# Performance work log

Measured on AMD Instinct MI355X. Metric: run time of the kernel, lower is better.

The kernel has to match this reference:

```python
import jax, jax.numpy as jnp
import numpy as np

D_MODEL = 1024
NUM_HEADS = 16
ROPE_THETA = 10000.0


def setup_inputs() -> dict:
    key = jax.random.key(0)
    ks = jax.random.split(key, 5)
    B, S, D = 4, 2048, D_MODEL
    scale = 1.0 / np.sqrt(D)
    return {
        "x": jax.random.normal(ks[0], (B, S, D), dtype=jnp.float32),
        "Wq": jax.random.normal(ks[1], (D, D), dtype=jnp.float32) * scale,
        "Wk": jax.random.normal(ks[2], (D, D), dtype=jnp.float32) * scale,
        "Wv": jax.random.normal(ks[3], (D, D), dtype=jnp.float32) * scale,
        "Wo": jax.random.normal(ks[4], (D, D), dtype=jnp.float32) * scale,
        "token_positions": jnp.arange(S, dtype=jnp.int32),
    }


def _rope(x, pos, theta=ROPE_THETA):
    # x: (b, h, s, d); interleaved-pair rotary embedding
    d = x.shape[-1]
    inv_freq = 1.0 / (theta ** (jnp.arange(0, d, 2, dtype=jnp.float32) / d))  # (d/2,)
    ang = pos.astype(jnp.float32)[:, None] * inv_freq[None, :]  # (s, d/2)
    cos, sin = jnp.cos(ang), jnp.sin(ang)
    x1, x2 = x[..., ::2], x[..., 1::2]
    out = jnp.stack([x1 * cos - x2 * sin, x1 * sin + x2 * cos], axis=-1)
    return out.reshape(x.shape)


def reference(x, Wq, Wk, Wv, Wo, token_positions):
    B, S, D = x.shape
    H = NUM_HEADS
    dh = D // H
    # torch nn.Linear(bias=False): y = x @ W.T
    q = jnp.einsum('bsd,ed->bse', x, Wq).reshape(B, S, H, dh).transpose(0, 2, 1, 3)
    k = jnp.einsum('bsd,ed->bse', x, Wk).reshape(B, S, H, dh).transpose(0, 2, 1, 3)
    v = jnp.einsum('bsd,ed->bse', x, Wv).reshape(B, S, H, dh).transpose(0, 2, 1, 3)
    q = _rope(q, token_positions)
    k = _rope(k, token_positions)
    scores = jnp.einsum('bhqd,bhkd->bhqk', q, k) / jnp.sqrt(jnp.array(dh, x.dtype))
    causal = jnp.tril(jnp.ones((S, S), dtype=bool))
    scores = jnp.where(causal, scores, jnp.array(-jnp.inf, scores.dtype))
    probs = jax.nn.softmax(scores, axis=-1)
    attn = jnp.einsum('bhqk,bhkd->bhqd', probs, v)  # (b, h, s, dh)
    attn = attn.transpose(0, 2, 1, 3).reshape(B, S, D)
    return jnp.einsum('bsd,ed->bse', attn, Wo)
```

## Files before the change

kernel.cpp:

```cpp
#include <hip/hip_runtime.h>
#include <hip/hip_bf16.h>
#include <stdint.h>

#define S_LEN 2048
#define BATCH 4
#define NH    16
#define DH    64
#define DM    1024
#define MTOT  (BATCH*S_LEN)

typedef short bf16x8 __attribute__((ext_vector_type(8)));
typedef float f32x4 __attribute__((ext_vector_type(4)));
typedef uint32_t u32x4 __attribute__((ext_vector_type(4)));

__device__ __forceinline__ uint16_t f2bf(float f) {
  union { float f; uint32_t i; } c; c.f = f;
  uint32_t r = c.i + 0x7fffu + ((c.i >> 16) & 1u);
  return (uint16_t)(r >> 16);
}
__device__ __forceinline__ float bf2f(uint16_t u) {
  union { uint32_t i; float f; } c; c.i = ((uint32_t)u) << 16; return c.f;
}

__device__ __forceinline__ uint32_t cvt_pk_bf16(float a, float b) {
  uint32_t r;
  asm("v_cvt_pk_bf16_f32 %0, %1, %2" : "=v"(r) : "v"(a), "v"(b));
  return r;
}

__device__ __forceinline__ void async_copy16(void* lds, const void* g) {
  __builtin_amdgcn_global_load_lds(
      (const __attribute__((address_space(1))) void*)g,
      (__attribute__((address_space(3))) void*)lds, 16, 0, 0);
}

__global__ __launch_bounds__(256) void cvt_f32_bf16(const float* __restrict__ in,
                                                    uint16_t* __restrict__ out, int n4) {
  int stride = gridDim.x * blockDim.x;
  for (int i = blockIdx.x * blockDim.x + threadIdx.x; i < n4; i += stride) {
    float4 v = ((const float4*)in)[i];
    ushort4 o;
    o.x = f2bf(v.x); o.y = f2bf(v.y); o.z = f2bf(v.z); o.w = f2bf(v.w);
    ((ushort4*)out)[i] = o;
  }
}

__global__ __launch_bounds__(256) void cvt_w4(const float* __restrict__ wq,
                                              const float* __restrict__ wk,
                                              const float* __restrict__ wv,
                                              const float* __restrict__ wo,
                                              uint16_t* __restrict__ out) {
  const int sel = blockIdx.y;
  const float* src = sel == 0 ? wq : sel == 1 ? wk : sel == 2 ? wv : wo;
  uint16_t* dst = out + (size_t)sel * DM * DM;
  const int n4 = DM * DM / 4;
  const int stride = gridDim.x * blockDim.x;
  for (int i = blockIdx.x * blockDim.x + threadIdx.x; i < n4; i += stride) {
    float4 v = ((const float4*)src)[i];
    ushort4 o;
    o.x = f2bf(v.x); o.y = f2bf(v.y); o.z = f2bf(v.z); o.w = f2bf(v.w);
    ((ushort4*)dst)[i] = o;
  }
}

template<int MODE, int BN>
__global__ __launch_bounds__(256) void gemm_bt(const uint16_t* __restrict__ A,
                                               const uint16_t* __restrict__ Bw,
                                               void* __restrict__ outp,
                                               const int* __restrict__ pos) {
  constexpr int K = DM;
  constexpr int NT = K / 32;
  constexpr int WC = BN / 2;
  constexpr int NF = WC / 16;
  __shared__ __align__(16) uint16_t lA[3][128 * 32];
  __shared__ __align__(16) uint16_t lB[3][BN * 32];
  const int tid = threadIdx.x;
  const int w = tid >> 6, lane = tid & 63;
  const int l15 = lane & 15, lhi = lane >> 4;
  const int wr = w >> 1, wc = w & 1;

  const int nx = gridDim.x, nwg = nx * gridDim.y;
  const int flat = blockIdx.y * nx + blockIdx.x;
  const int wg = (flat & 7) * (nwg >> 3) + (flat >> 3);
  const int bm = (wg / nx) * 128, bn = (wg % nx) * BN;

  const int srow = tid >> 2;
  const int cb = (tid & 3) * 16;

  auto stage = [&](int b, int t) {
    const int k0 = t * 32;
#pragma unroll
    for (int i = 0; i < 2; ++i)
      async_copy16((char*)lA[b] + i * 4096 + w * 1024,
                   (const char*)A + ((size_t)(bm + i * 64 + srow) * K + k0) * 2 + cb);
#pragma unroll
    for (int i = 0; i < BN / 64; ++i)
      async_copy16((char*)lB[b] + i * 4096 + w * 1024,
                   (const char*)Bw + ((size_t)(bn + i * 64 + srow) * K + k0) * 2 + cb);
  };

  f32x4 acc[4][NF] = {};

  stage(0, 0);
  stage(1, 1);
  if constexpr (BN == 128) asm volatile("s_waitcnt vmcnt(4)" ::: "memory");
  else                     asm volatile("s_waitcnt vmcnt(3)" ::: "memory");
  __builtin_amdgcn_s_barrier();
  __builtin_amdgcn_sched_barrier(0);

  int cur = 0;
  for (int t = 0; t < NT; ++t) {
    const bool pre = (t + 2 < NT);
    int bnext = cur + 2; if (bnext >= 3) bnext -= 3;
    if (pre) stage(bnext, t + 2);

    bf16x8 af[4], bfr[NF];
#pragma unroll
    for (int mf = 0; mf < 4; ++mf)
      af[mf] = *(const bf16x8*)((const char*)lA[cur] +
                                (wr * 64 + mf * 16 + l15) * 64 + lhi * 16);
#pragma unroll
    for (int nf = 0; nf < NF; ++nf)
      bfr[nf] = *(const bf16x8*)((const char*)lB[cur] +
                                 (wc * WC + nf * 16 + l15) * 64 + lhi * 16);
    __builtin_amdgcn_s_setprio(1);
#pragma unroll
    for (int mf = 0; mf < 4; ++mf)
#pragma unroll
      for (int nf = 0; nf < NF; ++nf)
        acc[mf][nf] = __builtin_amdgcn_mfma_f32_16x16x32_bf16(af[mf], bfr[nf], acc[mf][nf], 0, 0, 0);
    __builtin_amdgcn_s_setprio(0);

    if (pre) {
      if constexpr (BN == 128) asm volatile("s_waitcnt vmcnt(4)" ::: "memory");
      else                     asm volatile("s_waitcnt vmcnt(3)" ::: "memory");
    } else {
      asm volatile("s_waitcnt vmcnt(0)" ::: "memory");
    }
    __builtin_amdgcn_s_barrier();
    __builtin_amdgcn_sched_barrier(0);
    cur = cur + 1 == 3 ? 0 : cur + 1;
  }

  if (MODE == 0) {
    const int tsel = bn >> 10;
    uint16_t* out = (uint16_t*)outp + (size_t)tsel * ((size_t)MTOT * DM);
    if (tsel < 2) {
      const float l2t_32 = 0.41524101186092074f;
      const float qsc = tsel == 0 ? 0.18033688011112042f : 1.0f;
#pragma unroll
      for (int mf = 0; mf < 4; ++mf) {
        float ps[4];
#pragma unroll
        for (int r = 0; r < 4; ++r) {
          const int m = bm + wr * 64 + mf * 16 + lhi * 4 + r;
          ps[r] = (float)pos[m & (S_LEN - 1)];
        }
#pragma unroll
        for (int nf = 0; nf < NF; ++nf) {
          const int n = bn + wc * WC + nf * 16 + l15;
          const int e = n & 1023;
          const int h = e >> 6, d = e & 63;
          const float inv = __builtin_amdgcn_exp2f(-(float)(d >> 1) * l2t_32);
#pragma unroll
          for (int r = 0; r < 4; ++r) {
            const int m = bm + wr * 64 + mf * 16 + lhi * 4 + r;
            const int b = m >> 11, s = m & (S_LEN - 1);
            const float v = acc[mf][nf][r];
            const float p = __shfl_xor(v, 1);
            const float ang = ps[r] * inv;
            const float cs = __cosf(ang) * qsc, sn = __sinf(ang) * qsc;
            const float val = (l15 & 1) ? (p * sn + v * cs) : (v * cs - p * sn);
            out[(((size_t)(b * NH + h) * S_LEN + s) << 6) + d] = f2bf(val);
          }
        }
      }
    } else {
#pragma unroll
      for (int mf = 0; mf < 4; ++mf)
#pragma unroll
        for (int nf = 0; nf < NF; ++nf)
#pragma unroll
          for (int r = 0; r < 4; ++r) {
            const int m = bm + wr * 64 + mf * 16 + lhi * 4 + r;
            const int n = bn + wc * WC + nf * 16 + l15;
            const int b = m >> 11, s = m & (S_LEN - 1);
            const int e = n & 1023;
            const int h = e >> 6, d = e & 63;
            out[(((size_t)(b * NH + h) * S_LEN + s) << 6) + d] = f2bf(acc[mf][nf][r]);
          }
    }
  } else {
    float* out = (float*)outp;
#pragma unroll
    for (int mf = 0; mf < 4; ++mf)
#pragma unroll
      for (int nf = 0; nf < NF; ++nf)
#pragma unroll
        for (int r = 0; r < 4; ++r) {
          const int m = bm + wr * 64 + mf * 16 + lhi * 4 + r;
          const int n = bn + wc * WC + nf * 16 + l15;
          out[(size_t)m * DM + n] = acc[mf][nf][r];
        }
  }
}

__global__ __launch_bounds__(256) void transpose_v(const uint16_t* __restrict__ v,
                                                   uint16_t* __restrict__ vt) {
  __shared__ uint16_t t[64 * 65];
  const int bh = blockIdx.y, s0 = blockIdx.x * 64;
  const uint16_t* vb = v + (size_t)bh * S_LEN * 64 + (size_t)s0 * 64;
  uint16_t* ob = vt + (size_t)bh * 64 * S_LEN + s0;
  for (int o = threadIdx.x; o < 64 * 64; o += 256) {
    const int r = o >> 6, c = o & 63;
    t[c * 65 + r] = vb[(size_t)r * 64 + c];
  }
  __syncthreads();
  for (int o = threadIdx.x; o < 64 * 64; o += 256) {
    const int d = o >> 6, p = o & 63;
    const int sp = (p & 32) | (((p >> 2) & 3) << 3) | (((p >> 4) & 1) << 2) | (p & 3);
    ob[(size_t)d * S_LEN + sp] = t[d * 65 + p];
  }
}

__global__ __launch_bounds__(512, 4) void attn_kernel(const uint16_t* __restrict__ q,
                                                      const uint16_t* __restrict__ kk,
                                                      const uint16_t* __restrict__ vt,
                                                      uint16_t* __restrict__ o) {
  const int bh = blockIdx.y;
  const int p = blockIdx.x;
  const int tid = threadIdx.x;
  const int w = __builtin_amdgcn_readfirstlane(tid >> 6);
  const int lane = tid & 63;
  const int l15 = lane & 15, lhi = lane >> 4;
  const uint16_t* qb = q + (size_t)bh * S_LEN * DH;
  const uint16_t* kb = kk + (size_t)bh * S_LEN * DH;
  const uint16_t* vb = vt + (size_t)bh * DH * S_LEN;

  __shared__ uint16_t lK[2][128 * 64];
  __shared__ uint16_t lV[2][64 * 128];

  const int krow_l = lane >> 3;
  const int scK = (lane & 7) ^ krow_l;
  const int vrow_l = lane >> 4;

  auto stage = [&](int b, int t) {
    const int k0 = t * 128;
#pragma unroll
    for (int i = 0; i < 2; ++i) {
      const int krow = w * 16 + i * 8 + krow_l;
      async_copy16((char*)lK[b] + w * 2048 + i * 1024 + lane * 16,
                   (const char*)kb + ((size_t)(k0 + krow) * 64 + scK * 8) * 2);
      const int vd = w * 8 + i * 4 + vrow_l;
      const int scV = (lane & 15) ^ (vd & 15);
      async_copy16((char*)lV[b] + w * 2048 + i * 1024 + lane * 16,
                   (const char*)vb + ((size_t)vd * S_LEN + k0 + scV * 8) * 2);
    }
  };

  stage(0, 0);
  asm volatile("s_waitcnt vmcnt(0)" ::: "memory");
  __syncthreads();

  int cur = 0;
  const int b_out = bh >> 4, h_out = bh & 15;

  for (int s = 0; s < 2; ++s) {
    const int qtile = s ? p : (15 - p);
    const int q0 = qtile * 128 + w * 16;

    bf16x8 qf[2];
#pragma unroll
    for (int c = 0; c < 2; ++c)
      qf[c] = *(const bf16x8*)(qb + (size_t)(q0 + l15) * DH + c * 32 + lhi * 8);

    f32x4 oa[4] = {};
    float mr = -1e30f, lr = 0.f;

    const int nt = qtile + 1;
    for (int t = 0; t < nt; ++t) {
      if (t + 1 < nt) stage(cur ^ 1, t + 1);
      else if (s == 0) stage(cur ^ 1, 0);

      const bool diag = (t == qtile);
      const int fMf = diag ? w : 7;
      const int fE  = diag ? (w | 1) : 7;
      const int cE  = diag ? (w >> 1) : 3;

      f32x4 sf[8];
      __builtin_amdgcn_s_setprio(1);
#pragma unroll
      for (int f = 0; f < 8; ++f) {
        f32x4 z = {0.f, 0.f, 0.f, 0.f};
        if (f <= fMf) {
          const int kr = f * 16 + l15;
          const char* kbase = (const char*)lK[cur] + kr * 128;
          bf16x8 kf0 = *(const bf16x8*)(kbase + ((lhi ^ (kr & 7)) << 4));
          bf16x8 kf1 = *(const bf16x8*)(kbase + (((4 + lhi) ^ (kr & 7)) << 4));
          z = __builtin_amdgcn_mfma_f32_16x16x32_bf16(kf0, qf[0], z, 0, 0, 0);
          z = __builtin_amdgcn_mfma_f32_16x16x32_bf16(kf1, qf[1], z, 0, 0, 0);
        }
        sf[f] = z;
      }
      __builtin_amdgcn_s_setprio(0);

      if (diag) {
        const int qrow = q0 + l15;
        const int k0 = t * 128;
#pragma unroll
        for (int f = 0; f < 8; ++f)
          if (f <= fE)
#pragma unroll
            for (int r = 0; r < 4; ++r) {
              const int kv = k0 + f * 16 + lhi * 4 + r;
              if (kv > qrow) sf[f][r] = -1e30f;
            }
      }

      float pm = -1e30f;
#pragma unroll
      for (int f = 0; f < 8; ++f)
        if (f <= fE)
#pragma unroll
          for (int r = 0; r < 4; ++r) pm = fmaxf(pm, sf[f][r]);
      pm = fmaxf(pm, __shfl_xor(pm, 16));
      pm = fmaxf(pm, __shfl_xor(pm, 32));

      if (!__all(pm <= mr + 8.0f)) {
        const float mn = fmaxf(mr, pm);
        const float resc = __builtin_amdgcn_exp2f(mr - mn);
        mr = mn;
        lr *= resc;
#pragma unroll
        for (int r = 0; r < 4; ++r) {
          const float rb = __shfl(resc, (lhi << 2) + r);
#pragma unroll
          for (int df = 0; df < 4; ++df) oa[df][r] *= rb;
        }
      }

      float rs = 0.f;
#pragma unroll
      for (int f = 0; f < 8; ++f)
        if (f <= fE)
#pragma unroll
          for (int r = 0; r < 4; ++r) {
            const float pv = __builtin_amdgcn_exp2f(sf[f][r] - mr);
            sf[f][r] = pv;
            rs += pv;
          }
      rs += __shfl_xor(rs, 16);
      rs += __shfl_xor(rs, 32);
      lr += rs;

#pragma unroll
      for (int c = 0; c < 4; ++c) {
        if (c <= cE) {
          u32x4 u;
          u.x = cvt_pk_bf16(sf[2 * c][0], sf[2 * c][1]);
          u.y = cvt_pk_bf16(sf[2 * c][2], sf[2 * c][3]);
          u.z = cvt_pk_bf16(sf[2 * c + 1][0], sf[2 * c + 1][1]);
          u.w = cvt_pk_bf16(sf[2 * c + 1][2], sf[2 * c + 1][3]);
          bf16x8 pa = __builtin_bit_cast(bf16x8, u);
          __builtin_amdgcn_s_setprio(1);
#pragma unroll
          for (int df = 0; df < 4; ++df) {
            const int vr = df * 16 + l15;
            bf16x8 vf = *(const bf16x8*)((const char*)lV[cur] + vr * 256 +
                                         ((((c << 2) + lhi) ^ (vr & 15)) << 4));
            oa[df] = __builtin_amdgcn_mfma_f32_16x16x32_bf16(pa, vf, oa[df], 0, 0, 0);
          }
          __builtin_amdgcn_s_setprio(0);
        }
      }

      asm volatile("s_waitcnt vmcnt(0)" ::: "memory");
      __syncthreads();
      cur ^= 1;
    }

    float inv[4];
#pragma unroll
    for (int r = 0; r < 4; ++r)
      inv[r] = __builtin_amdgcn_rcpf(__shfl(lr, (lhi << 2) + r));
#pragma unroll
    for (int df = 0; df < 4; ++df)
#pragma unroll
      for (int r = 0; r < 4; ++r) {
        const int srow_o = q0 + lhi * 4 + r;
        const float val = oa[df][r] * inv[r];
        const int d = df * 16 + l15;
        o[((size_t)(b_out * S_LEN + srow_o)) * DM + h_out * 64 + d] = f2bf(val);
      }
  }
}

extern "C" void kernel_launch(void* const* d_in, const int* in_sizes, int n_in,
                              void* d_out, int out_size, void* d_ws, size_t ws_size,
                              hipStream_t stream) {
  const float* x = (const float*)d_in[0];
  const float* Wq = (const float*)d_in[1];
  const float* Wk = (const float*)d_in[2];
  const float* Wv = (const float*)d_in[3];
  const float* Wo = (const float*)d_in[4];
  const int* pos = (const int*)d_in[5];

  char* ws = (char*)d_ws;
  size_t off = 0;
  auto alloc = [&](size_t bytes) {
    void* p = ws + off;
    off += (bytes + 255) & ~(size_t)255;
    return p;
  };
  uint16_t* xb    = (uint16_t*)alloc((size_t)MTOT * DM * 2);
  uint16_t* wqkvb = (uint16_t*)alloc((size_t)4 * DM * DM * 2);
  uint16_t* qkvb  = (uint16_t*)alloc((size_t)3 * MTOT * DM * 2);
  uint16_t* vtb   = (uint16_t*)alloc((size_t)MTOT * DM * 2);
  uint16_t* wob = wqkvb + (size_t)3 * DM * DM;
  uint16_t* qb = qkvb;
  uint16_t* kbuf = qkvb + (size_t)MTOT * DM;
  uint16_t* vbuf = qkvb + (size_t)2 * MTOT * DM;
  uint16_t* attnb = xb;

  cvt_f32_bf16<<<2048, 256, 0, stream>>>(x, xb, MTOT * DM / 4);
  cvt_w4<<<dim3(128, 4), 256, 0, stream>>>(Wq, Wk, Wv, Wo, wqkvb);

  gemm_bt<0, 128><<<dim3(24, MTOT / 128), 256, 0, stream>>>(xb, wqkvb, qkvb, pos);

  transpose_v<<<dim3(32, 64), 256, 0, stream>>>(vbuf, vtb);

  attn_kernel<<<dim3(8, 64), 512, 0, stream>>>(qb, kbuf, vtb, attnb);

  gemm_bt<1, 64><<<dim3(16, MTOT / 128), 256, 0, stream>>>(attnb, wob, d_out, nullptr);
}
```

Measured before the change: 176.4 us.

## Enlarge GEMM tiles to 128x256 with BK=64, XOR-swizzled LDS, double buffering

Reworks the projection GEMM to use 512-thread blocks computing 128x256 output tiles with a K-step of 64. The LDS layout gets an XOR swizzle of 16-byte chunks to avoid bank conflicts. The triple-buffer pipeline with fine-grained vmcnt waits becomes a simple double buffer synchronised by __syncthreads. The aim is more data reuse per block and fewer LDS conflicts. The cost is fewer blocks: the output projection drops to 256 blocks, and the coarser synchronisation may expose more load latency.

```diff
diff --git a/kernel.cpp b/kernel.cpp
--- a/kernel.cpp
+++ b/kernel.cpp
@@ -63,83 +63,84 @@
   }
 }
 
-template<int MODE, int BN>
-__global__ __launch_bounds__(256) void gemm_bt(const uint16_t* __restrict__ A,
+template<int MODE>
+__global__ __launch_bounds__(512) void gemm_bt(const uint16_t* __restrict__ A,
                                                const uint16_t* __restrict__ Bw,
                                                void* __restrict__ outp,
                                                const int* __restrict__ pos) {
   constexpr int K = DM;
-  constexpr int NT = K / 32;
-  constexpr int WC = BN / 2;
-  constexpr int NF = WC / 16;
-  __shared__ __align__(16) uint16_t lA[3][128 * 32];
-  __shared__ __align__(16) uint16_t lB[3][BN * 32];
+  constexpr int NT = K / 64;
+  __shared__ __align__(16) uint16_t lA[2][128 * 64];
+  __shared__ __align__(16) uint16_t lB[2][256 * 64];
   const int tid = threadIdx.x;
   const int w = tid >> 6, lane = tid & 63;
   const int l15 = lane & 15, lhi = lane >> 4;
-  const int wr = w >> 1, wc = w & 1;
+  const int wr = w >> 2, wc = w & 3;
 
   const int nx = gridDim.x, nwg = nx * gridDim.y;
   const int flat = blockIdx.y * nx + blockIdx.x;
   const int wg = (flat & 7) * (nwg >> 3) + (flat >> 3);
-  const int bm = (wg / nx) * 128, bn = (wg % nx) * BN;
-
-  const int srow = tid >> 2;
-  const int cb = (tid & 3) * 16;
+  const int bm = (wg / nx) * 128, bn = (wg % nx) * 256;
 
   auto stage = [&](int b, int t) {
-    const int k0 = t * 32;
-#pragma unroll
-    for (int i = 0; i < 2; ++i)
-      async_copy16((char*)lA[b] + i * 4096 + w * 1024,
-                   (const char*)A + ((size_t)(bm + i * 64 + srow) * K + k0) * 2 + cb);
-#pragma unroll
-    for (int i = 0; i < BN / 64; ++i)
-      async_copy16((char*)lB[b] + i * 4096 + w * 1024,
-                   (const char*)Bw + ((size_t)(bn + i * 64 + srow) * K + k0) * 2 + cb);
+    const int k0 = t * 64;
+#pragma unroll
+    for (int j = 0; j < 2; ++j) {
+      const int c = j * 512 + tid;
+      const int row = c >> 3, cir = c & 7;
+      const int gc = cir ^ (row & 7);
+      async_copy16((char*)lA[b] + c * 16,
+                   (const char*)A + ((size_t)(bm + row) * K + k0 + gc * 8) * 2);
+    }
+#pragma unroll
+    for (int j = 0; j < 4; ++j) {
+      const int c = j * 512 + tid;
+      const int row = c >> 3, cir = c & 7;
+      const int gc = cir ^ (row & 7);
+      async_copy16((char*)lB[b] + c * 16,
+                   (const char*)Bw + ((size_t)(bn + row) * K + k0 + gc * 8) * 2);
+    }
   };
 
-  f32x4 acc[4][NF] = {};
+  f32x4 acc[4][4] = {};
 
   stage(0, 0);
-  stage(1, 1);
-  if constexpr (BN == 128) asm volatile("s_waitcnt vmcnt(4)" ::: "memory");
-  else                     asm volatile("s_waitcnt vmcnt(3)" ::: "memory");
-  __builtin_amdgcn_s_barrier();
-  __builtin_amdgcn_sched_barrier(0);
+  __syncthreads();
 
   int cur = 0;
   for (int t = 0; t < NT; ++t) {
-    const bool pre = (t + 2 < NT);
-    int bnext = cur + 2; if (bnext >= 3) bnext -= 3;
-    if (pre) stage(bnext, t + 2);
-
-    bf16x8 af[4], bfr[NF];
+    if (t + 1 < NT) stage(cur ^ 1, t + 1);
+
+    bf16x8 af[4][2], bfr[4][2];
+#pragma unroll
+    for (int mf = 0; mf < 4; ++mf) {
+      const int ar = wr * 64 + mf * 16 + l15;
+#pragma unroll
+      for (int kc = 0; kc < 2; ++kc)
+        af[mf][kc] = *(const bf16x8*)((const char*)lA[cur] + ar * 128 +
+                                      (((kc * 4 + lhi) ^ (ar & 7)) << 4));
+    }
+#pragma unroll
+    for (int nf = 0; nf < 4; ++nf) {
+      const int br = wc * 64 + nf * 16 + l15;
+#pragma unroll
+      for (int kc = 0; kc < 2; ++kc)
+        bfr[nf][kc] = *(const bf16x8*)((const char*)lB[cur] + br * 128 +
+                                       (((kc * 4 + lhi) ^ (br & 7)) << 4));
+    }
+    __builtin_amdgcn_s_setprio(1);
 #pragma unroll
     for (int mf = 0; mf < 4; ++mf)
-      af[mf] = *(const bf16x8*)((const char*)lA[cur] +
-                                (wr * 64 + mf * 16 + l15) * 64 + lhi * 16);
-#pragma unroll
-    for (int nf = 0; nf < NF; ++nf)
-      bfr[nf] = *(const bf16x8*)((const char*)lB[cur] +
-                                 (wc * WC + nf * 16 + l15) * 64 + lhi * 16);
-    __builtin_amdgcn_s_setprio(1);
-#pragma unroll
-    for (int mf = 0; mf < 4; ++mf)
-#pragma unroll
-      for (int nf = 0; nf < NF; ++nf)
-        acc[mf][nf] = __builtin_amdgcn_mfma_f32_16x16x32_bf16(af[mf], bfr[nf], acc[mf][nf], 0, 0, 0);
+#pragma unroll
+      for (int nf = 0; nf < 4; ++nf)
+#pragma unroll
+        for (int kc = 0; kc < 2; ++kc)
+          acc[mf][nf] = __builtin_amdgcn_mfma_f32_16x16x32_bf16(
+              af[mf][kc], bfr[nf][kc], acc[mf][nf], 0, 0, 0);
     __builtin_amdgcn_s_setprio(0);
 
-    if (pre) {
-      if constexpr (BN == 128) asm volatile("s_waitcnt vmcnt(4)" ::: "memory");
-      else                     asm volatile("s_waitcnt vmcnt(3)" ::: "memory");
-    } else {
-      asm volatile("s_waitcnt vmcnt(0)" ::: "memory");
-    }
-    __builtin_amdgcn_s_barrier();
-    __builtin_amdgcn_sched_barrier(0);
-    cur = cur + 1 == 3 ? 0 : cur + 1;
+    __syncthreads();
+    cur ^= 1;
   }
 
   if (MODE == 0) {
@@ -157,8 +158,8 @@
           ps[r] = (float)pos[m & (S_LEN - 1)];
         }
 #pragma unroll
-        for (int nf = 0; nf < NF; ++nf) {
-          const int n = bn + wc * WC + nf * 16 + l15;
+        for (int nf = 0; nf < 4; ++nf) {
+          const int n = bn + wc * 64 + nf * 16 + l15;
           const int e = n & 1023;
           const int h = e >> 6, d = e & 63;
           const float inv = __builtin_amdgcn_exp2f(-(float)(d >> 1) * l2t_32);
@@ -179,11 +180,11 @@
 #pragma unroll
       for (int mf = 0; mf < 4; ++mf)
 #pragma unroll
-        for (int nf = 0; nf < NF; ++nf)
+        for (int nf = 0; nf < 4; ++nf)
 #pragma unroll
           for (int r = 0; r < 4; ++r) {
             const int m = bm + wr * 64 + mf * 16 + lhi * 4 + r;
-            const int n = bn + wc * WC + nf * 16 + l15;
+            const int n = bn + wc * 64 + nf * 16 + l15;
             const int b = m >> 11, s = m & (S_LEN - 1);
             const int e = n & 1023;
             const int h = e >> 6, d = e & 63;
@@ -195,11 +196,11 @@
 #pragma unroll
     for (int mf = 0; mf < 4; ++mf)
 #pragma unroll
-      for (int nf = 0; nf < NF; ++nf)
+      for (int nf = 0; nf < 4; ++nf)
 #pragma unroll
         for (int r = 0; r < 4; ++r) {
           const int m = bm + wr * 64 + mf * 16 + lhi * 4 + r;
-          const int n = bn + wc * WC + nf * 16 + l15;
+          const int n = bn + wc * 64 + nf * 16 + l15;
           out[(size_t)m * DM + n] = acc[mf][nf][r];
         }
   }
@@ -425,11 +426,11 @@
   cvt_f32_bf16<<<2048, 256, 0, stream>>>(x, xb, MTOT * DM / 4);
   cvt_w4<<<dim3(128, 4), 256, 0, stream>>>(Wq, Wk, Wv, Wo, wqkvb);
 
-  gemm_bt<0, 128><<<dim3(24, MTOT / 128), 256, 0, stream>>>(xb, wqkvb, qkvb, pos);
+  gemm_bt<0><<<dim3(12, MTOT / 128), 512, 0, stream>>>(xb, wqkvb, qkvb, pos);
 
   transpose_v<<<dim3(32, 64), 256, 0, stream>>>(vbuf, vtb);
 
   attn_kernel<<<dim3(8, 64), 512, 0, stream>>>(qb, kbuf, vtb, attnb);
 
-  gemm_bt<1, 64><<<dim3(16, MTOT / 128), 256, 0, stream>>>(attnb, wob, d_out, nullptr);
-}
+  gemm_bt<1><<<dim3(4, MTOT / 128), 512, 0, stream>>>(attnb, wob, d_out, nullptr);
+}
```

Measured after the change: 178.1 us. No clear change (+1.0%).

## Process two query tiles per wave to reuse each staged K/V tile

Applied to the files above, without the earlier changes.

Each attention block now handles a 256-row query span as two 128-row sub-tiles, so every K/V tile staged into LDS feeds two sets of score and PV MFMAs instead of one. This halves the global-to-LDS K/V traffic and barrier count per query row. In exchange the grid is halved to 256 blocks, register use roughly doubles for accumulators and softmax state (launch bounds relaxed to 2 blocks per CU), and the causal load balance is coarser.

```diff
diff --git a/kernel.cpp b/kernel.cpp
--- a/kernel.cpp
+++ b/kernel.cpp
@@ -223,7 +223,7 @@
   }
 }
 
-__global__ __launch_bounds__(512, 4) void attn_kernel(const uint16_t* __restrict__ q,
+__global__ __launch_bounds__(512, 2) void attn_kernel(const uint16_t* __restrict__ q,
                                                       const uint16_t* __restrict__ kk,
                                                       const uint16_t* __restrict__ vt,
                                                       uint16_t* __restrict__ o) {
@@ -266,111 +266,118 @@
   const int b_out = bh >> 4, h_out = bh & 15;
 
   for (int s = 0; s < 2; ++s) {
-    const int qtile = s ? p : (15 - p);
-    const int q0 = qtile * 128 + w * 16;
-
-    bf16x8 qf[2];
-#pragma unroll
-    for (int c = 0; c < 2; ++c)
-      qf[c] = *(const bf16x8*)(qb + (size_t)(q0 + l15) * DH + c * 32 + lhi * 8);
-
-    f32x4 oa[4] = {};
-    float mr = -1e30f, lr = 0.f;
-
-    const int nt = qtile + 1;
+    const int j = s ? p : (7 - p);
+    const int qbase = j * 256;
+
+    bf16x8 qf[2][2];
+#pragma unroll
+    for (int fr = 0; fr < 2; ++fr)
+#pragma unroll
+      for (int c = 0; c < 2; ++c)
+        qf[fr][c] = *(const bf16x8*)(qb + (size_t)(qbase + fr * 128 + w * 16 + l15) * DH +
+                                     c * 32 + lhi * 8);
+
+    f32x4 oa[2][4] = {};
+    float mr[2] = {-1e30f, -1e30f}, lr[2] = {0.f, 0.f};
+
+    const int nt = 2 * j + 2;
     for (int t = 0; t < nt; ++t) {
       if (t + 1 < nt) stage(cur ^ 1, t + 1);
       else if (s == 0) stage(cur ^ 1, 0);
 
-      const bool diag = (t == qtile);
-      const int fMf = diag ? w : 7;
-      const int fE  = diag ? (w | 1) : 7;
-      const int cE  = diag ? (w >> 1) : 3;
-
-      f32x4 sf[8];
-      __builtin_amdgcn_s_setprio(1);
-#pragma unroll
-      for (int f = 0; f < 8; ++f) {
-        f32x4 z = {0.f, 0.f, 0.f, 0.f};
-        if (f <= fMf) {
-          const int kr = f * 16 + l15;
-          const char* kbase = (const char*)lK[cur] + kr * 128;
-          bf16x8 kf0 = *(const bf16x8*)(kbase + ((lhi ^ (kr & 7)) << 4));
-          bf16x8 kf1 = *(const bf16x8*)(kbase + (((4 + lhi) ^ (kr & 7)) << 4));
-          z = __builtin_amdgcn_mfma_f32_16x16x32_bf16(kf0, qf[0], z, 0, 0, 0);
-          z = __builtin_amdgcn_mfma_f32_16x16x32_bf16(kf1, qf[1], z, 0, 0, 0);
-        }
-        sf[f] = z;
-      }
-      __builtin_amdgcn_s_setprio(0);
-
-      if (diag) {
-        const int qrow = q0 + l15;
-        const int k0 = t * 128;
+#pragma unroll
+      for (int fr = 0; fr < 2; ++fr) {
+        if (fr == 0 && t == nt - 1) continue;
+        const bool diag = (t == 2 * j + fr);
+        const int fMf = diag ? w : 7;
+        const int fE  = diag ? (w | 1) : 7;
+        const int cE  = diag ? (w >> 1) : 3;
+        const int q0 = qbase + fr * 128 + w * 16;
+
+        f32x4 sf[8];
+        __builtin_amdgcn_s_setprio(1);
+#pragma unroll
+        for (int f = 0; f < 8; ++f) {
+          f32x4 z = {0.f, 0.f, 0.f, 0.f};
+          if (f <= fMf) {
+            const int kr = f * 16 + l15;
+            const char* kbase = (const char*)lK[cur] + kr * 128;
+            bf16x8 kf0 = *(const bf16x8*)(kbase + ((lhi ^ (kr & 7)) << 4));
+            bf16x8 kf1 = *(const bf16x8*)(kbase + (((4 + lhi) ^ (kr & 7)) << 4));
+            z = __builtin_amdgcn_mfma_f32_16x16x32_bf16(kf0, qf[fr][0], z, 0, 0, 0);
+            z = __builtin_amdgcn_mfma_f32_16x16x32_bf16(kf1, qf[fr][1], z, 0, 0, 0);
+          }
+          sf[f] = z;
+        }
+        __builtin_amdgcn_s_setprio(0);
+
+        if (diag) {
+          const int qrow = w * 16 + l15;
+#pragma unroll
+          for (int f = 0; f < 8; ++f)
+            if (f <= fE)
+#pragma unroll
+              for (int r = 0; r < 4; ++r) {
+                const int kv = f * 16 + lhi * 4 + r;
+                if (kv > qrow) sf[f][r] = -1e30f;
+              }
+        }
+
+        float pm = -1e30f;
 #pragma unroll
         for (int f = 0; f < 8; ++f)
           if (f <= fE)
 #pragma unroll
+            for (int r = 0; r < 4; ++r) pm = fmaxf(pm, sf[f][r]);
+        pm = fmaxf(pm, __shfl_xor(pm, 16));
+        pm = fmaxf(pm, __shfl_xor(pm, 32));
+
+        if (!__all(pm <= mr[fr] + 8.0f)) {
+          const float mn = fmaxf(mr[fr], pm);
+          const float resc = __builtin_amdgcn_exp2f(mr[fr] - mn);
+          mr[fr] = mn;
+          lr[fr] *= resc;
+#pragma unroll
+          for (int r = 0; r < 4; ++r) {
+            const float rb = __shfl(resc, (lhi << 2) + r);
+#pragma unroll
+            for (int df = 0; df < 4; ++df) oa[fr][df][r] *= rb;
+          }
+        }
+
+        float rs = 0.f;
+#pragma unroll
+        for (int f = 0; f < 8; ++f)
+          if (f <= fE)
+#pragma unroll
             for (int r = 0; r < 4; ++r) {
-              const int kv = k0 + f * 16 + lhi * 4 + r;
-              if (kv > qrow) sf[f][r] = -1e30f;
+              const float pv = __builtin_amdgcn_exp2f(sf[f][r] - mr[fr]);
+              sf[f][r] = pv;
+              rs += pv;
             }
-      }
-
-      float pm = -1e30f;
-#pragma unroll
-      for (int f = 0; f < 8; ++f)
-        if (f <= fE)
-#pragma unroll
-          for (int r = 0; r < 4; ++r) pm = fmaxf(pm, sf[f][r]);
-      pm = fmaxf(pm, __shfl_xor(pm, 16));
-      pm = fmaxf(pm, __shfl_xor(pm, 32));
-
-      if (!__all(pm <= mr + 8.0f)) {
-        const float mn = fmaxf(mr, pm);
-        const float resc = __builtin_amdgcn_exp2f(mr - mn);
-        mr = mn;
-        lr *= resc;
-#pragma unroll
-        for (int r = 0; r < 4; ++r) {
-          const float rb = __shfl(resc, (lhi << 2) + r);
-#pragma unroll
-          for (int df = 0; df < 4; ++df) oa[df][r] *= rb;
-        }
-      }
-
-      float rs = 0.f;
-#pragma unroll
-      for (int f = 0; f < 8; ++f)
-        if (f <= fE)
-#pragma unroll
-          for (int r = 0; r < 4; ++r) {
-            const float pv = __builtin_amdgcn_exp2f(sf[f][r] - mr);
-            sf[f][r] = pv;
-            rs += pv;
+        rs += __shfl_xor(rs, 16);
+        rs += __shfl_xor(rs, 32);
+        lr[fr] += rs;
+
+#pragma unroll
+        for (int c = 0; c < 4; ++c) {
+          if (c <= cE) {
+            u32x4 u;
+            u.x = cvt_pk_bf16(sf[2 * c][0], sf[2 * c][1]);
+            u.y = cvt_pk_bf16(sf[2 * c][2], sf[2 * c][3]);
+            u.z = cvt_pk_bf16(sf[2 * c + 1][0], sf[2 * c + 1][1]);
+            u.w = cvt_pk_bf16(sf[2 * c + 1][2], sf[2 * c + 1][3]);
+            bf16x8 pa = __builtin_bit_cast(bf16x8, u);
+            __builtin_amdgcn_s_setprio(1);
+#pragma unroll
+            for (int df = 0; df < 4; ++df) {
+              const int vr = df * 16 + l15;
+              bf16x8 vf = *(const bf16x8*)((const char*)lV[cur] + vr * 256 +
+                                           ((((c << 2) + lhi) ^ (vr & 15)) << 4));
+              oa[fr][df] = __builtin_amdgcn_mfma_f32_16x16x32_bf16(pa, vf, oa[fr][df], 0, 0, 0);
+            }
+            __builtin_amdgcn_s_setprio(0);
           }
-      rs += __shfl_xor(rs, 16);
-      rs += __shfl_xor(rs, 32);
-      lr += rs;
-
-#pragma unroll
-      for (int c = 0; c < 4; ++c) {
-        if (c <= cE) {
-          u32x4 u;
-          u.x = cvt_pk_bf16(sf[2 * c][0], sf[2 * c][1]);
-          u.y = cvt_pk_bf16(sf[2 * c][2], sf[2 * c][3]);
-          u.z = cvt_pk_bf16(sf[2 * c + 1][0], sf[2 * c + 1][1]);
-          u.w = cvt_pk_bf16(sf[2 * c + 1][2], sf[2 * c + 1][3]);
-          bf16x8 pa = __builtin_bit_cast(bf16x8, u);
-          __builtin_amdgcn_s_setprio(1);
-#pragma unroll
-          for (int df = 0; df < 4; ++df) {
-            const int vr = df * 16 + l15;
-            bf16x8 vf = *(const bf16x8*)((const char*)lV[cur] + vr * 256 +
-                                         ((((c << 2) + lhi) ^ (vr & 15)) << 4));
-            oa[df] = __builtin_amdgcn_mfma_f32_16x16x32_bf16(pa, vf, oa[df], 0, 0, 0);
-          }
-          __builtin_amdgcn_s_setprio(0);
         }
       }
 
@@ -379,19 +386,23 @@
       cur ^= 1;
     }
 
-    float inv[4];
-#pragma unroll
-    for (int r = 0; r < 4; ++r)
-      inv[r] = __builtin_amdgcn_rcpf(__shfl(lr, (lhi << 2) + r));
-#pragma unroll
-    for (int df = 0; df < 4; ++df)
-#pragma unroll
-      for (int r = 0; r < 4; ++r) {
-        const int srow_o = q0 + lhi * 4 + r;
-        const float val = oa[df][r] * inv[r];
-        const int d = df * 16 + l15;
-        o[((size_t)(b_out * S_LEN + srow_o)) * DM + h_out * 64 + d] = f2bf(val);
-      }
+#pragma unroll
+    for (int fr = 0; fr < 2; ++fr) {
+      const int q0 = qbase + fr * 128 + w * 16;
+      float inv[4];
+#pragma unroll
+      for (int r = 0; r < 4; ++r)
+        inv[r] = __builtin_amdgcn_rcpf(__shfl(lr[fr], (lhi << 2) + r));
+#pragma unroll
+      for (int df = 0; df < 4; ++df)
+#pragma unroll
+        for (int r = 0; r < 4; ++r) {
+          const int srow_o = q0 + lhi * 4 + r;
+          const float val = oa[fr][df][r] * inv[r];
+          const int d = df * 16 + l15;
+          o[((size_t)(b_out * S_LEN + srow_o)) * DM + h_out * 64 + d] = f2bf(val);
+        }
+    }
   }
 }
 
@@ -429,7 +440,7 @@
 
   transpose_v<<<dim3(32, 64), 256, 0, stream>>>(vbuf, vtb);
 
-  attn_kernel<<<dim3(8, 64), 512, 0, stream>>>(qb, kbuf, vtb, attnb);
+  attn_kernel<<<dim3(4, 64), 512, 0, stream>>>(qb, kbuf, vtb, attnb);
 
   gemm_bt<1, 64><<<dim3(16, MTOT / 128), 256, 0, stream>>>(attnb, wob, d_out, nullptr);
 }
```

Result: slower. 193.2 us (+9.6%).
